# Optimization experiments

Measured on AMD Instinct MI355X. Metric: run time of the kernel, lower is better.

Reference implementation:

```python
import jax, jax.numpy as jnp
import numpy as np

N = 8192
E = 262144
IN_DIM = 128
OUT_DIM = 16


def _linear_params(key, fan_in, fan_out):
    k1, k2 = jax.random.split(key)
    bound = 1.0 / np.sqrt(fan_in)
    W = jax.random.uniform(k1, (fan_in, fan_out), jnp.float32, -bound, bound)
    b = jax.random.uniform(k2, (fan_out,), jnp.float32, -bound, bound)
    return W, b


def setup_inputs() -> dict:
    key = jax.random.key(0)
    ks = jax.random.split(key, 10)
    x = jax.random.normal(ks[0], (N, IN_DIM), jnp.float32)
    edge_index = jax.random.randint(ks[1], (2, E), 0, N, jnp.int64)
    W1, b1 = _linear_params(ks[2], IN_DIM, 128)
    W2, b2 = _linear_params(ks[3], 128, 256)
    W3, b3 = _linear_params(ks[4], 256, 64)
    Wk, bk = _linear_params(ks[5], 256, 256)
    Wq, bq = _linear_params(ks[6], 256, 256)
    Wr, br = _linear_params(ks[7], IN_DIM, 64)
    Wf, bf = _linear_params(ks[8], 64, OUT_DIM)
    ln_g = jnp.ones((64,), jnp.float32)
    ln_b = jnp.zeros((64,), jnp.float32)
    return dict(x=x, edge_index=edge_index, W1=W1, b1=b1, W2=W2, b2=b2,
                W3=W3, b3=b3, Wk=Wk, bk=bk, Wq=Wq, bq=bq, Wr=Wr, br=br,
                ln_g=ln_g, ln_b=ln_b, Wf=Wf, bf=bf)


def gcn_conv(x, W, b, row, col, n):
    # PyG GCNConv: add self-loops, symmetric normalization, aggregate src->dst
    xw = x @ W                                          # [N, F_out]
    loops = jnp.arange(n, dtype=row.dtype)
    r = jnp.concatenate([row, loops])
    c = jnp.concatenate([col, loops])
    deg = jax.ops.segment_sum(jnp.ones_like(c, jnp.float32), c, num_segments=n)
    dinv = jnp.where(deg > 0, jax.lax.rsqrt(jnp.maximum(deg, 1e-12)), 0.0)
    norm = dinv[r] * dinv[c]                            # [E+N]
    out = jax.ops.segment_sum(norm[:, None] * xw[r], c, num_segments=n)
    return out + b


def _forward(x, edge_index, W1, b1, W2, b2, W3, b3, Wk, bk, Wq, bq,
             Wr, br, ln_g, ln_b, Wf, bf):
    row, col = edge_index[0], edge_index[1]
    n = x.shape[0]
    residual = x @ Wr + br                              # [N, 64]
    h = jax.nn.leaky_relu(gcn_conv(x, W1, b1, row, col, n))   # dropout = eval no-op
    h = jax.nn.leaky_relu(gcn_conv(h, W2, b2, row, col, n))   # [N, 256]
    keys = h @ Wk + bk
    queries = h @ Wq + bq
    scores = queries @ keys.T                           # [N, N] dense, as in source
    mask = jnp.zeros((n, n), jnp.float32).at[row, col].set(1.0)
    scores = scores * mask                              # multiplicative mask (faithful)
    attn = jax.nn.softmax(scores, axis=-1)
    h = attn @ h                                        # [N, 256]
    h = jax.nn.leaky_relu(gcn_conv(h, W3, b3, row, col, n))   # [N, 64]
    z = h + residual
    mu = jnp.mean(z, axis=-1, keepdims=True)
    var = jnp.mean((z - mu) ** 2, axis=-1, keepdims=True)
    z = (z - mu) * jax.lax.rsqrt(var + 1e-5) * ln_g + ln_b
    pooled = jnp.max(z, axis=0)                         # 'max' pooling -> [64]
    return pooled @ Wf + bf                             # [OUT_DIM]


def reference(x, edge_index, W1, b1, W2, b2, W3, b3, Wk, bk, Wq, bq,
              Wr, br, ln_g, ln_b, Wf, bf):
    return _forward(x, edge_index, W1, b1, W2, b2, W3, b3, Wk, bk, Wq, bq,
                    Wr, br, ln_g, ln_b, Wf, bf)
```

## Files before the change

### kernel.cpp

```cpp
#include <hip/hip_runtime.h>
#include <hip/hip_fp16.h>
#include <cstdint>
#include <cstddef>

#define NNODES 8192
#define NEDGES 262144
#define MAXDEG 96
#define SMEM_BYTES 10496

typedef _Float16 f16x8 __attribute__((ext_vector_type(8)));
typedef _Float16 h2v   __attribute__((ext_vector_type(2)));
typedef float    f32x4 __attribute__((ext_vector_type(4)));

__device__ __forceinline__ float leaky(float v){ return v > 0.f ? v : 0.01f*v; }

__device__ __forceinline__ unsigned fmap(float f){
  unsigned u = __float_as_uint(f);
  return (u & 0x80000000u) ? ~u : (u | 0x80000000u);
}
__device__ __forceinline__ float funmap(unsigned u){
  return (u & 0x80000000u) ? __uint_as_float(u & 0x7FFFFFFFu) : __uint_as_float(~u);
}
__device__ __forceinline__ h2v as_h2(unsigned u){
  union{ unsigned x; h2v h; } c; c.x = u; return c.h;
}

struct GP {
  const float *x; const int *ei;
  const float *W1,*b1,*W2,*b2,*W3,*b3,*Wk,*bk,*Wq,*bq,*Wr,*br,*lng,*lnb,*Wf,*bfv;
  float* out;
  __half *xw1h,*h1h,*h1ah,*h2h,*qth,*gh,*hw3h;
  float *resid,*sw3;
  __half *Wqkt,*W2t,*W3t;
  float *bqk,*wb,*s0p;
  int *degc,*degr,*csrc,*csrd;
  unsigned* poolpart;
};

__device__ __forceinline__ void gemm_tile(const __half* __restrict__ A,
    const __half* __restrict__ Bt, const float* __restrict__ bias,
    float* __restrict__ Cf, __half* __restrict__ Ch, float* __restrict__ csum,
    int K, int N, int act, int bx, int by,
    _Float16 (*As)[40], _Float16 (*Bs)[40], float* cs){
  int t = threadIdx.x, w = t>>6, lane = t&63;
  int m0 = bx*64, n0 = by*64;
  int quad = lane>>4, l15 = lane&15;
  int srow = t>>2, soff = (t&3)*8;
  f32x4 acc0 = {0.f,0.f,0.f,0.f}, acc1 = acc0, acc2 = acc0, acc3 = acc0;
  for (int k0 = 0; k0 < K; k0 += 32){
    *(uint4*)&As[srow][soff] = *(const uint4*)(A  + (size_t)(m0+srow)*K + k0 + soff);
    *(uint4*)&Bs[srow][soff] = *(const uint4*)(Bt + (size_t)(n0+srow)*K + k0 + soff);
    __syncthreads();
    f16x8 af = *(const f16x8*)&As[w*16 + l15][quad*8];
    f16x8 b0 = *(const f16x8*)&Bs[ 0 + l15][quad*8];
    f16x8 b1 = *(const f16x8*)&Bs[16 + l15][quad*8];
    f16x8 b2 = *(const f16x8*)&Bs[32 + l15][quad*8];
    f16x8 b3 = *(const f16x8*)&Bs[48 + l15][quad*8];
    acc0 = __builtin_amdgcn_mfma_f32_16x16x32_f16(af, b0, acc0, 0,0,0);
    acc1 = __builtin_amdgcn_mfma_f32_16x16x32_f16(af, b1, acc1, 0,0,0);
    acc2 = __builtin_amdgcn_mfma_f32_16x16x32_f16(af, b2, acc2, 0,0,0);
    acc3 = __builtin_amdgcn_mfma_f32_16x16x32_f16(af, b3, acc3, 0,0,0);
    __syncthreads();
  }
  f32x4 accs[4] = {acc0, acc1, acc2, acc3};
  if (csum){
    if (t < 64) cs[t] = 0.f;
    __syncthreads();
    #pragma unroll
    for (int nt=0; nt<4; ++nt){
      float pp = accs[nt][0]+accs[nt][1]+accs[nt][2]+accs[nt][3];
      atomicAdd(&cs[nt*16 + l15], pp);
    }
    __syncthreads();
    if (t < 64) atomicAdd(&csum[n0 + t], cs[t]);
  }
  #pragma unroll
  for (int nt=0; nt<4; ++nt){
    int col = n0 + nt*16 + l15;
    float bv = bias ? bias[col] : 0.f;
    #pragma unroll
    for (int r=0;r<4;r++){
      int row = m0 + w*16 + quad*4 + r;
      float v = accs[nt][r] + bv;
      if (act) v = leaky(v);
      if (Cf) Cf[(size_t)row*N + col] = v;
      if (Ch) Ch[(size_t)row*N + col] = __float2half(v);
    }
  }
}

template<int TRANSB>
__device__ __forceinline__ void gemm_f32(const float* __restrict__ A,
    const float* __restrict__ B, const float* __restrict__ bias,
    float* __restrict__ Cf, __half* __restrict__ Ch,
    int K, int N, int bx, int by,
    _Float16 (*As)[40], _Float16 (*Bs)[40]){
  int t = threadIdx.x, w = t>>6, lane = t&63;
  int m0 = bx*64, n0 = by*64;
  int quad = lane>>4, l15 = lane&15;
  int srow = t>>2, soff = (t&3)*8;
  f32x4 acc0 = {0.f,0.f,0.f,0.f}, acc1 = acc0, acc2 = acc0, acc3 = acc0;
  for (int k0 = 0; k0 < K; k0 += 32){
    float4 a0 = *(const float4*)(A + (size_t)(m0+srow)*K + k0 + soff);
    float4 a1 = *(const float4*)(A + (size_t)(m0+srow)*K + k0 + soff + 4);
    _Float16* ad = &As[srow][soff];
    ad[0]=(_Float16)a0.x; ad[1]=(_Float16)a0.y; ad[2]=(_Float16)a0.z; ad[3]=(_Float16)a0.w;
    ad[4]=(_Float16)a1.x; ad[5]=(_Float16)a1.y; ad[6]=(_Float16)a1.z; ad[7]=(_Float16)a1.w;
    _Float16* bd = &Bs[srow][soff];
    if (TRANSB){
      #pragma unroll
      for (int u=0;u<8;u++)
        bd[u] = (_Float16)B[(size_t)(k0+soff+u)*N + n0+srow];
    } else {
      float4 b0 = *(const float4*)(B + (size_t)(n0+srow)*K + k0 + soff);
      float4 b1 = *(const float4*)(B + (size_t)(n0+srow)*K + k0 + soff + 4);
      bd[0]=(_Float16)b0.x; bd[1]=(_Float16)b0.y; bd[2]=(_Float16)b0.z; bd[3]=(_Float16)b0.w;
      bd[4]=(_Float16)b1.x; bd[5]=(_Float16)b1.y; bd[6]=(_Float16)b1.z; bd[7]=(_Float16)b1.w;
    }
    __syncthreads();
    f16x8 af = *(const f16x8*)&As[w*16 + l15][quad*8];
    f16x8 b0 = *(const f16x8*)&Bs[ 0 + l15][quad*8];
    f16x8 b1 = *(const f16x8*)&Bs[16 + l15][quad*8];
    f16x8 b2 = *(const f16x8*)&Bs[32 + l15][quad*8];
    f16x8 b3 = *(const f16x8*)&Bs[48 + l15][quad*8];
    acc0 = __builtin_amdgcn_mfma_f32_16x16x32_f16(af, b0, acc0, 0,0,0);
    acc1 = __builtin_amdgcn_mfma_f32_16x16x32_f16(af, b1, acc1, 0,0,0);
    acc2 = __builtin_amdgcn_mfma_f32_16x16x32_f16(af, b2, acc2, 0,0,0);
    acc3 = __builtin_amdgcn_mfma_f32_16x16x32_f16(af, b3, acc3, 0,0,0);
    __syncthreads();
  }
  f32x4 accs[4] = {acc0, acc1, acc2, acc3};
  #pragma unroll
  for (int nt=0; nt<4; ++nt){
    int col = n0 + nt*16 + l15;
    float bv = bias ? bias[col] : 0.f;
    #pragma unroll
    for (int r=0;r<4;r++){
      int row = m0 + w*16 + quad*4 + r;
      float v = accs[nt][r] + bv;
      if (Cf) Cf[(size_t)row*N + col] = v;
      if (Ch) Ch[(size_t)row*N + col] = __float2half(v);
    }
  }
}

template<int INS, int OUTS, int ACT>
__device__ __forceinline__ void agg128w(const __half* __restrict__ in,
    const int* __restrict__ deg, const int* __restrict__ src,
    __half* __restrict__ outp, const float* __restrict__ bias, int i){
  int lane = threadIdx.x & 63;
  int dcc = deg[i];
  float dc = rsqrtf((float)(dcc+1));
  int e0 = i*MAXDEG, e1 = e0 + dcc;
  float2 acc = make_float2(0.f, 0.f);
  for (int eb = e0; eb < e1; eb += 8){
    int m = e1 - eb; if (m > 8) m = 8;
    int r[8];
    #pragma unroll
    for (int u=0;u<8;u++) r[u] = src[(u<m) ? eb+u : eb];
    __half2 hv[8]; float sc[8];
    #pragma unroll
    for (int u=0;u<8;u++){
      hv[u] = *(const __half2*)(in + (size_t)r[u]*128 + lane*2);
      sc[u] = INS ? 1.f : rsqrtf((float)(deg[r[u]]+1));
    }
    #pragma unroll
    for (int u=0;u<8;u++){
      if (u < m){
        float2 h = __half22float2(hv[u]);
        if (INS){ acc.x += h.x; acc.y += h.y; }
        else { acc.x = fmaf(sc[u], h.x, acc.x); acc.y = fmaf(sc[u], h.y, acc.y); }
      }
    }
  }
  float2 self = __half22float2(*(const __half2*)(in + (size_t)i*128 + lane*2));
  float ss = INS ? 1.f : dc;
  float ox = dc*(ss*self.x + acc.x);
  float oy = dc*(ss*self.y + acc.y);
  if (ACT){
    ox = leaky(ox + bias[lane*2]);
    oy = leaky(oy + bias[lane*2+1]);
  }
  if (OUTS){ ox *= dc; oy *= dc; }
  *(__half2*)(outp + (size_t)i*128 + lane*2) = __floats2half2_rn(ox, oy);
}

__device__ __forceinline__ void attn_unit(const GP& p, int u){
  const int n = NNODES;
  int w = threadIdx.x>>6, lane = threadIdx.x&63;
  int i = u*4 + w;
  int fo = lane*4;
  uint2 qtu = *(const uint2*)(p.qth + (size_t)i*256 + fo);
  h2v q0 = as_h2(qtu.x), q1 = as_h2(qtu.y);
  float4 wbv = *(const float4*)(p.wb + fo);
  uint2 hiu  = *(const uint2*)(p.h2h + (size_t)i*256 + fo);
  float2 hia = __half22float2(*(__half2*)&hiu.x);
  float2 hib = __half22float2(*(__half2*)&hiu.y);
  float pv = hia.x*wbv.x + hia.y*wbv.y + hib.x*wbv.z + hib.y*wbv.w;
  #pragma unroll
  for (int mm=32; mm; mm>>=1) pv += __shfl_xor(pv, mm, 64);
  float base = pv + p.s0p[0];
  int dri = p.degr[i];
  int e0 = i*MAXDEG, e1 = e0 + dri;
  float acc = 0.f, dsum = 0.f;
  int slot = lane & 7;
  for (int eb = e0; eb < e1; eb += 8){
    int m = e1 - eb; if (m > 8) m = 8;
    int j[8];
    #pragma unroll
    for (int u8=0;u8<8;u8++) j[u8] = p.csrd[(u8<m) ? eb+u8 : eb];
    uint2 hv[8]; float gv[8];
    #pragma unroll
    for (int u8=0;u8<8;u8++){
      hv[u8] = *(const uint2*)(p.h2h + (size_t)j[u8]*256 + fo);
      gv[u8] = __half2float(p.gh[(size_t)j[u8]*64 + lane]);
    }
    float d[8];
    #pragma unroll
    for (int u8=0;u8<8;u8++)
      d[u8] = __builtin_amdgcn_fdot2(q1, as_h2(hv[u8].y),
              __builtin_amdgcn_fdot2(q0, as_h2(hv[u8].x), 0.f, false), false);
    #pragma unroll
    for (int v=0;v<8;v++) d[v] += __shfl_xor(d[v], 1, 64);
    float e0_ = (lane&1) ? d[1] : d[0];
    float e1_ = (lane&1) ? d[3] : d[2];
    float e2_ = (lane&1) ? d[5] : d[4];
    float e3_ = (lane&1) ? d[7] : d[6];
    e0_ += __shfl_xor(e0_, 2, 64);  e1_ += __shfl_xor(e1_, 2, 64);
    e2_ += __shfl_xor(e2_, 2, 64);  e3_ += __shfl_xor(e3_, 2, 64);
    float f0_ = (lane&2) ? e1_ : e0_;
    float f1_ = (lane&2) ? e3_ : e2_;
    f0_ += __shfl_xor(f0_, 4, 64);  f1_ += __shfl_xor(f1_, 4, 64);
    float g_ = (lane&4) ? f1_ : f0_;
    g_ += __shfl_xor(g_,  8, 64);
    g_ += __shfl_xor(g_, 16, 64);
    g_ += __shfl_xor(g_, 32, 64);
    float wep = __expf(g_ + base);
    float wm = (slot < m) ? wep : 0.f;
    wm += __shfl_xor(wm, 1, 64);
    wm += __shfl_xor(wm, 2, 64);
    wm += __shfl_xor(wm, 4, 64);
    dsum += wm;
    #pragma unroll
    for (int u8=0;u8<8;u8++){
      if (u8 < m){
        float wu = __shfl(wep, u8, 64);
        acc = fmaf(wu - 1.f, gv[u8], acc);
      }
    }
  }
  float inv = 1.0f / ((float)(n - dri) + dsum);
  float di = rsqrtf((float)(p.degc[i]+1));
  p.hw3h[(size_t)i*64 + lane] = __float2half(di * (p.sw3[lane] + acc) * inv);
}

__device__ __forceinline__ void zp_wave(const GP& p, int c){
  int lane = threadIdx.x & 63;
  int dcc = p.degc[c];
  float dc = rsqrtf((float)(dcc+1));
  float acc = 0.f;
  int e0 = c*MAXDEG, e1 = e0 + dcc;
  for (int eb = e0; eb < e1; eb += 8){
    int m = e1 - eb; if (m > 8) m = 8;
    int r[8];
    #pragma unroll
    for (int u=0;u<8;u++) r[u] = p.csrc[(u<m) ? eb+u : eb];
    __half hval[8];
    #pragma unroll
    for (int u=0;u<8;u++) hval[u] = p.hw3h[(size_t)r[u]*64 + lane];
    #pragma unroll
    for (int u=0;u<8;u++)
      if (u < m) acc += __half2float(hval[u]);
  }
  float self = __half2float(p.hw3h[(size_t)c*64 + lane]);
  float v = leaky(dc*(self + acc) + p.b3[lane]) + p.resid[(size_t)c*64 + lane];
  float s = v;
  #pragma unroll
  for (int mm=32; mm; mm>>=1) s += __shfl_xor(s, mm, 64);
  float mu = s * (1.0f/64.0f);
  float d = v - mu;
  float s2 = d*d;
  #pragma unroll
  for (int mm=32; mm; mm>>=1) s2 += __shfl_xor(s2, mm, 64);
  float zv = d * rsqrtf(s2*(1.0f/64.0f) + 1e-5f) * p.lng[lane] + p.lnb[lane];
  atomicMax(&p.poolpart[(c & 63)*64 + lane], fmap(zv));
}

__device__ __forceinline__ void final_unit(const GP& p, char* smem){
  int t = threadIdx.x, f = t & 63, g = t >> 6;
  unsigned (*sm)[64] = (unsigned(*)[64])smem;
  float* pool = (float*)(smem + 1024);
  unsigned mu = 0u;
  for (int b = g; b < 64; b += 4) mu = max(mu, p.poolpart[b*64 + f]);
  sm[g][f] = mu;
  __syncthreads();
  if (g == 0)
    pool[f] = funmap(max(max(sm[0][f],sm[1][f]), max(sm[2][f],sm[3][f])));
  __syncthreads();
  if (t < 16){
    float a = p.bfv[t];
    #pragma unroll
    for (int ff=0; ff<64; ++ff) a = fmaf(pool[ff], p.Wf[ff*16 + t], a);
    p.out[t] = a;
  }
}

__global__ __launch_bounds__(256) void k_z(GP p){
  int idx = blockIdx.x*256 + threadIdx.x;
  int4 z = {0,0,0,0};
  ((int4*)p.degc)[idx] = z;
}

__global__ __launch_bounds__(256) void k_pre(GP p){
  __shared__ __align__(16) char smem[SMEM_BYTES];
  _Float16 (*As)[40] = (_Float16(*)[40])smem;
  _Float16 (*Bs)[40] = (_Float16(*)[40])(smem + 5120);
  int b = blockIdx.x, t = threadIdx.x;
  if (b < 1024){
    int e = b*256 + t;
    int r = p.ei[e], c = p.ei[NEDGES+e];
    int p1 = atomicAdd(&p.degc[c],1); p.csrc[c*MAXDEG + p1] = r;
    int p2 = atomicAdd(&p.degr[r],1); p.csrd[r*MAXDEG + p2] = c;
  } else if (b < 1280){
    int bb = b - 1024;
    gemm_f32<1>(p.x, p.W1, nullptr, nullptr, p.xw1h, 128, 128, bb>>1, bb&1, As, Bs);
  } else if (b < 1296){
    int bb = b - 1280;
    gemm_f32<0>(p.Wk, p.Wq, nullptr, nullptr, p.Wqkt, 256, 256, bb&3, bb>>2, As, Bs);
  } else if (b < 1424){
    gemm_f32<1>(p.x, p.Wr, p.br, p.resid, nullptr, 128, 64, b-1296, 0, As, Bs);
  } else if (b < 1552){
    int idx = (b-1424)*256 + t;
    int nn = idx >> 7, k = idx & 127;
    p.W2t[idx] = __float2half(p.W2[k*256 + nn]);
  } else if (b < 1616){
    int idx = (b-1552)*256 + t;
    int nn = idx >> 8, k = idx & 255;
    p.W3t[idx] = __float2half(p.W3[k*64 + nn]);
  } else if (b < 1632){
    p.poolpart[(b-1616)*256 + t] = 0u;
  } else if (b == 1632){
    if (t < 64) p.sw3[t] = 0.f;
  } else {
    int c = b - 1633;
    float* ra = (float*)smem; float* rb = ra + 256; float* rc = rb + 256;
    ra[t] = p.Wk[c*256 + t] * p.bq[t];
    rb[t] = p.Wq[c*256 + t] * p.bk[t];
    if (c == 0) rc[t] = p.bq[t]*p.bk[t];
    __syncthreads();
    for (int off=128; off; off>>=1){
      if (t < off){
        ra[t] += ra[t+off];
        rb[t] += rb[t+off];
        if (c == 0) rc[t] += rc[t+off];
      }
      __syncthreads();
    }
    if (t == 0){
      p.bqk[c] = ra[0];
      p.wb[c]  = rb[0];
      if (c == 0) p.s0p[0] = rc[0];
    }
  }
}

__global__ __launch_bounds__(256) void k_agg0(GP p){
  int i = blockIdx.x*4 + (threadIdx.x>>6);
  agg128w<0,1,1>(p.xw1h, p.degc, p.csrc, p.h1h, p.b1, i);
}
__global__ __launch_bounds__(256) void k_agg1(GP p){
  int i = blockIdx.x*4 + (threadIdx.x>>6);
  agg128w<1,0,0>(p.h1h, p.degc, p.csrc, p.h1ah, nullptr, i);
}

__global__ __launch_bounds__(256) void k_gemm2(GP p){
  __shared__ __align__(16) char smem[SMEM_BYTES];
  _Float16 (*As)[40] = (_Float16(*)[40])smem;
  _Float16 (*Bs)[40] = (_Float16(*)[40])(smem + 5120);
  int b = blockIdx.x;
  gemm_tile(p.h1ah, p.W2t, p.b2, nullptr, p.h2h, nullptr, 128, 256, 1, b>>2, b&3, As, Bs, nullptr);
}

__global__ __launch_bounds__(256) void k_mix2(GP p){
  __shared__ __align__(16) char smem[SMEM_BYTES];
  _Float16 (*As)[40] = (_Float16(*)[40])smem;
  _Float16 (*Bs)[40] = (_Float16(*)[40])(smem + 5120);
  float* cs = (float*)(smem + 10240);
  int b = blockIdx.x;
  if (b < 128) gemm_tile(p.h2h, p.W3t, nullptr, nullptr, p.gh, p.sw3, 256, 64, 0, b, 0, As, Bs, cs);
  else {
    int bb = b - 128;
    gemm_tile(p.h2h, p.Wqkt, p.bqk, nullptr, p.qth, nullptr, 256, 256, 0, bb>>2, bb&3, As, Bs, cs);
  }
}

__global__ __launch_bounds__(256) void k_attn(GP p){ attn_unit(p, blockIdx.x); }

__global__ __launch_bounds__(256) void k_zp(GP p){
  int c = blockIdx.x*4 + (threadIdx.x>>6);
  zp_wave(p, c);
}

__global__ __launch_bounds__(256) void k_final(GP p){
  __shared__ __align__(16) char smem[SMEM_BYTES];
  final_unit(p, smem);
}

extern "C" void kernel_launch(void* const* d_in, const int* in_sizes, int n_in,
                              void* d_out, int out_size, void* d_ws, size_t ws_size,
                              hipStream_t stream){
  const int n = NNODES, E = NEDGES;
  char* ws = (char*)d_ws; size_t off = 0;
  auto alloc = [&](size_t bytes)->void*{
    void* pp = ws + off; off += (bytes + 255) & ~(size_t)255; return pp;
  };
  GP p;
  p.x   = (const float*)d_in[0];
  p.ei  = (const int*)d_in[1];
  p.W1  = (const float*)d_in[2];  p.b1 = (const float*)d_in[3];
  p.W2  = (const float*)d_in[4];  p.b2 = (const float*)d_in[5];
  p.W3  = (const float*)d_in[6];  p.b3 = (const float*)d_in[7];
  p.Wk  = (const float*)d_in[8];  p.bk = (const float*)d_in[9];
  p.Wq  = (const float*)d_in[10]; p.bq = (const float*)d_in[11];
  p.Wr  = (const float*)d_in[12]; p.br = (const float*)d_in[13];
  p.lng = (const float*)d_in[14]; p.lnb = (const float*)d_in[15];
  p.Wf  = (const float*)d_in[16]; p.bfv = (const float*)d_in[17];
  p.out = (float*)d_out;

  p.degc = (int*)alloc((size_t)n*4);
  p.degr = (int*)alloc((size_t)n*4);
  p.xw1h = (__half*)alloc((size_t)n*128*2);
  p.h1h  = (__half*)alloc((size_t)n*128*2);
  p.h1ah = (__half*)alloc((size_t)n*128*2);
  p.h2h  = (__half*)alloc((size_t)n*256*2);
  p.qth  = (__half*)alloc((size_t)n*256*2);
  p.gh   = (__half*)alloc((size_t)n*64*2);
  p.hw3h = (__half*)alloc((size_t)n*64*2);
  p.resid= (float*)alloc((size_t)n*64*4);
  p.sw3  = (float*)alloc(64*4);
  p.Wqkt = (__half*)alloc(256*256*2);
  p.W2t  = (__half*)alloc(128*256*2);
  p.W3t  = (__half*)alloc(256*64*2);
  p.bqk  = (float*)alloc(256*4);
  p.wb   = (float*)alloc(256*4);
  p.s0p  = (float*)alloc(4);
  p.csrc = (int*)alloc((size_t)n*MAXDEG*4);
  p.csrd = (int*)alloc((size_t)n*MAXDEG*4);
  p.poolpart = (unsigned*)alloc(64*64*4);

  k_z    <<<dim3(16),   256, 0, stream>>>(p);
  k_pre  <<<dim3(1889), 256, 0, stream>>>(p);
  k_agg0 <<<dim3(n/4),  256, 0, stream>>>(p);
  k_agg1 <<<dim3(n/4),  256, 0, stream>>>(p);
  k_gemm2<<<dim3(512),  256, 0, stream>>>(p);
  k_mix2 <<<dim3(640),  256, 0, stream>>>(p);
  k_attn <<<dim3(n/4),  256, 0, stream>>>(p);
  k_zp   <<<dim3(n/4),  256, 0, stream>>>(p);
  k_final<<<dim3(1),    256, 0, stream>>>(p);
}
```

Baseline: 204.9 us.

## Fuse layer-2 GCN aggregation with W2 GEMM and move weight prep into k_z

Replaces the separate layer-2 aggregation kernel and the W2 GEMM kernel with one kernel. Each block aggregates 32 nodes' neighbour features into shared memory, then multiplies that tile by W2 with MFMA, so the intermediate aggregated buffer never goes to global memory and one launch is dropped. Weight transposes, buffer zeroing and bias-product reductions move from k_pre into k_z. The trade-off is fewer blocks (256) for the fused step, each with a serial gather phase, which may lower occupancy and latency hiding.

```diff
diff --git a/kernel.cpp b/kernel.cpp
--- a/kernel.cpp
+++ b/kernel.cpp
@@ -29,7 +29,7 @@
   const float *x; const int *ei;
   const float *W1,*b1,*W2,*b2,*W3,*b3,*Wk,*bk,*Wq,*bq,*Wr,*br,*lng,*lnb,*Wf,*bfv;
   float* out;
-  __half *xw1h,*h1h,*h1ah,*h2h,*qth,*gh,*hw3h;
+  __half *xw1h,*h1h,*h2h,*qth,*gh,*hw3h;
   float *resid,*sw3;
   __half *Wqkt,*W2t,*W3t;
   float *bqk,*wb,*s0p;
@@ -306,9 +306,45 @@
 }
 
 __global__ __launch_bounds__(256) void k_z(GP p){
-  int idx = blockIdx.x*256 + threadIdx.x;
-  int4 z = {0,0,0,0};
-  ((int4*)p.degc)[idx] = z;
+  __shared__ float smv[768];
+  int b = blockIdx.x, t = threadIdx.x;
+  if (b < 16){
+    int idx = b*256 + t;
+    int4 z = {0,0,0,0};
+    ((int4*)p.degc)[idx] = z;
+  } else if (b < 144){
+    int idx = (b-16)*256 + t;
+    int nn = idx >> 7, k = idx & 127;
+    p.W2t[idx] = __float2half(p.W2[k*256 + nn]);
+  } else if (b < 208){
+    int idx = (b-144)*256 + t;
+    int nn = idx >> 8, k = idx & 255;
+    p.W3t[idx] = __float2half(p.W3[k*64 + nn]);
+  } else if (b < 224){
+    p.poolpart[(b-208)*256 + t] = 0u;
+  } else if (b == 224){
+    if (t < 64) p.sw3[t] = 0.f;
+  } else {
+    int c = b - 225;
+    float* ra = smv; float* rb = smv + 256; float* rc = smv + 512;
+    ra[t] = p.Wk[c*256 + t] * p.bq[t];
+    rb[t] = p.Wq[c*256 + t] * p.bk[t];
+    if (c == 0) rc[t] = p.bq[t]*p.bk[t];
+    __syncthreads();
+    for (int off=128; off; off>>=1){
+      if (t < off){
+        ra[t] += ra[t+off];
+        rb[t] += rb[t+off];
+        if (c == 0) rc[t] += rc[t+off];
+      }
+      __syncthreads();
+    }
+    if (t == 0){
+      p.bqk[c] = ra[0];
+      p.wb[c]  = rb[0];
+      if (c == 0) p.s0p[0] = rc[0];
+    }
+  }
 }
 
 __global__ __launch_bounds__(256) void k_pre(GP p){
@@ -327,40 +363,8 @@
   } else if (b < 1296){
     int bb = b - 1280;
     gemm_f32<0>(p.Wk, p.Wq, nullptr, nullptr, p.Wqkt, 256, 256, bb&3, bb>>2, As, Bs);
-  } else if (b < 1424){
+  } else {
     gemm_f32<1>(p.x, p.Wr, p.br, p.resid, nullptr, 128, 64, b-1296, 0, As, Bs);
-  } else if (b < 1552){
-    int idx = (b-1424)*256 + t;
-    int nn = idx >> 7, k = idx & 127;
-    p.W2t[idx] = __float2half(p.W2[k*256 + nn]);
-  } else if (b < 1616){
-    int idx = (b-1552)*256 + t;
-    int nn = idx >> 8, k = idx & 255;
-    p.W3t[idx] = __float2half(p.W3[k*64 + nn]);
-  } else if (b < 1632){
-    p.poolpart[(b-1616)*256 + t] = 0u;
-  } else if (b == 1632){
-    if (t < 64) p.sw3[t] = 0.f;
-  } else {
-    int c = b - 1633;
-    float* ra = (float*)smem; float* rb = ra + 256; float* rc = rb + 256;
-    ra[t] = p.Wk[c*256 + t] * p.bq[t];
-    rb[t] = p.Wq[c*256 + t] * p.bk[t];
-    if (c == 0) rc[t] = p.bq[t]*p.bk[t];
-    __syncthreads();
-    for (int off=128; off; off>>=1){
-      if (t < off){
-        ra[t] += ra[t+off];
-        rb[t] += rb[t+off];
-        if (c == 0) rc[t] += rc[t+off];
-      }
-      __syncthreads();
-    }
-    if (t == 0){
-      p.bqk[c] = ra[0];
-      p.wb[c]  = rb[0];
-      if (c == 0) p.s0p[0] = rc[0];
-    }
   }
 }
 
@@ -368,17 +372,66 @@
   int i = blockIdx.x*4 + (threadIdx.x>>6);
   agg128w<0,1,1>(p.xw1h, p.degc, p.csrc, p.h1h, p.b1, i);
 }
-__global__ __launch_bounds__(256) void k_agg1(GP p){
-  int i = blockIdx.x*4 + (threadIdx.x>>6);
-  agg128w<1,0,0>(p.h1h, p.degc, p.csrc, p.h1ah, nullptr, i);
-}
-
-__global__ __launch_bounds__(256) void k_gemm2(GP p){
-  __shared__ __align__(16) char smem[SMEM_BYTES];
-  _Float16 (*As)[40] = (_Float16(*)[40])smem;
-  _Float16 (*Bs)[40] = (_Float16(*)[40])(smem + 5120);
-  int b = blockIdx.x;
-  gemm_tile(p.h1ah, p.W2t, p.b2, nullptr, p.h2h, nullptr, 128, 256, 1, b>>2, b&3, As, Bs, nullptr);
+
+__global__ __launch_bounds__(256) void k_ag2(GP p){
+  __shared__ _Float16 h1a[32][136];
+  __shared__ _Float16 Bs2[256][40];
+  int t = threadIdx.x, w = t>>6, lane = t&63;
+  int base = blockIdx.x*32;
+  for (int q=0; q<8; ++q){
+    int i = base + w*8 + q;
+    int dcc = p.degc[i];
+    float dc = rsqrtf((float)(dcc+1));
+    int e0 = i*MAXDEG, e1 = e0 + dcc;
+    float2 acc = make_float2(0.f, 0.f);
+    for (int eb=e0; eb<e1; eb+=8){
+      int m = e1-eb; if (m>8) m=8;
+      int r[8];
+      #pragma unroll
+      for (int u=0;u<8;u++) r[u] = p.csrc[(u<m)?eb+u:eb];
+      __half2 hv[8];
+      #pragma unroll
+      for (int u=0;u<8;u++) hv[u] = *(const __half2*)(p.h1h + (size_t)r[u]*128 + lane*2);
+      #pragma unroll
+      for (int u=0;u<8;u++){
+        if (u<m){ float2 h=__half22float2(hv[u]); acc.x+=h.x; acc.y+=h.y; }
+      }
+    }
+    float2 self = __half22float2(*(const __half2*)(p.h1h + (size_t)i*128 + lane*2));
+    *(__half2*)&h1a[w*8+q][lane*2] = __floats2half2_rn(dc*(self.x+acc.x), dc*(self.y+acc.y));
+  }
+  __syncthreads();
+  int quad = lane>>4, l15 = lane&15;
+  int rg = w&1, ch = w>>1;
+  f32x4 acc[8];
+  #pragma unroll
+  for (int nt=0;nt<8;++nt) acc[nt] = (f32x4){0.f,0.f,0.f,0.f};
+  for (int k0=0;k0<128;k0+=32){
+    #pragma unroll
+    for (int pp=0;pp<4;pp++){
+      int row = pp*64 + (t>>2);
+      *(uint4*)&Bs2[row][(t&3)*8] = *(const uint4*)(p.W2t + (size_t)row*128 + k0 + (t&3)*8);
+    }
+    __syncthreads();
+    f16x8 af = *(const f16x8*)&h1a[rg*16 + l15][k0 + quad*8];
+    #pragma unroll
+    for (int nt=0; nt<8; ++nt){
+      f16x8 bf = *(const f16x8*)&Bs2[ch*128 + nt*16 + l15][quad*8];
+      acc[nt] = __builtin_amdgcn_mfma_f32_16x16x32_f16(af, bf, acc[nt], 0,0,0);
+    }
+    __syncthreads();
+  }
+  #pragma unroll
+  for (int nt=0;nt<8;++nt){
+    int col = ch*128 + nt*16 + l15;
+    float bv = p.b2[col];
+    #pragma unroll
+    for (int r=0;r<4;r++){
+      int row = base + rg*16 + quad*4 + r;
+      float v = leaky(acc[nt][r] + bv);
+      p.h2h[(size_t)row*256 + col] = __float2half(v);
+    }
+  }
 }
 
 __global__ __launch_bounds__(256) void k_mix2(GP p){
@@ -431,7 +484,6 @@
   p.degr = (int*)alloc((size_t)n*4);
   p.xw1h = (__half*)alloc((size_t)n*128*2);
   p.h1h  = (__half*)alloc((size_t)n*128*2);
-  p.h1ah = (__half*)alloc((size_t)n*128*2);
   p.h2h  = (__half*)alloc((size_t)n*256*2);
   p.qth  = (__half*)alloc((size_t)n*256*2);
   p.gh   = (__half*)alloc((size_t)n*64*2);
@@ -448,11 +500,10 @@
   p.csrd = (int*)alloc((size_t)n*MAXDEG*4);
   p.poolpart = (unsigned*)alloc(64*64*4);
 
-  k_z    <<<dim3(16),   256, 0, stream>>>(p);
-  k_pre  <<<dim3(1889), 256, 0, stream>>>(p);
+  k_z    <<<dim3(481),  256, 0, stream>>>(p);
+  k_pre  <<<dim3(1424), 256, 0, stream>>>(p);
   k_agg0 <<<dim3(n/4),  256, 0, stream>>>(p);
-  k_agg1 <<<dim3(n/4),  256, 0, stream>>>(p);
-  k_gemm2<<<dim3(512),  256, 0, stream>>>(p);
+  k_ag2  <<<dim3(n/32), 256, 0, stream>>>(p);
   k_mix2 <<<dim3(640),  256, 0, stream>>>(p);
   k_attn <<<dim3(n/4),  256, 0, stream>>>(p);
   k_zp   <<<dim3(n/4),  256, 0, stream>>>(p);
```

Measured after the change: 226.8 us. 1.11x slower.
